# Kernel tuning notes

Measured on AMD Instinct MI355X. Metric: run time of the kernel, lower is better.

## Reference

```python
import jax, jax.numpy as jnp
import numpy as np

# fixed finite-difference stencils (torch cross-correlation taps)
W5 = (1.0/12.0, -8.0/12.0, 0.0, 8.0/12.0, -1.0/12.0)  # five-point, pad=2
W3 = (-0.5, 0.0, 0.5)                                   # three-point, pad=1
P_LIST = np.array([10.0, 8.5, 5.0], dtype=np.float32).reshape(3, 1, 1)


def _circ_deriv(x, axis, taps, pad):
    # torch conv with circular pad: out[i] = sum_k w[k] * x[(i + k - pad) % n]
    # x[(i + k - pad) % n] == roll(x, pad - k)[i]
    out = jnp.zeros_like(x)
    for k, w in enumerate(taps):
        if w != 0.0:
            out = out + w * jnp.roll(x, pad - k, axis=axis)
    return out


def setup_inputs() -> dict:
    key = jax.random.key(0)
    k1, k2, k3, k4 = jax.random.split(key, 4)
    b, si_z, i_y, i_x = 4, 12, 720, 1440
    return {
        "Field": jax.random.normal(k1, (b, si_z, i_y, i_x), dtype=jnp.float32),
        "W": jax.random.normal(k2, (15, 12), dtype=jnp.float32) * 0.02,
        "b_bias": jax.random.normal(k3, (15,), dtype=jnp.float32) * 0.02,
        "thermal_factor": jax.random.normal(k4, (1,), dtype=jnp.float32),
    }


def reference(Field, W, b_bias, thermal_factor):
    b, si_z, i_y, i_x = Field.shape
    s = 4
    i_z = si_z // s  # == 3

    # backbone: 1x1 conv / channel-mixing linear, (b,12,y,x) -> (b,15,y,x)
    ml = jnp.einsum("oc,bcyx->boyx", W, Field) + b_bias[None, :, None, None]
    ml = ml.reshape(b, s + 1, i_z, i_y, i_x)
    ExternalForce = ml[:, :4]           # (b,4,z,y,x)
    o = ml[:, 4:5]                      # (b,1,z,y,x)

    F5 = Field.reshape(b, s, i_z, i_y, i_x)
    u = F5[:, 0:1]
    v = F5[:, 1:2]
    T = F5[:, 2:3]

    Fdx = _circ_deriv(F5, -1, W5, 2)    # d/dx, circular five-point
    Fdy = _circ_deriv(F5, -2, W5, 2)    # d/dy
    Fdz = _circ_deriv(F5, -3, W3, 1)    # d/dz, three-point

    p_list = jnp.asarray(P_LIST)        # (3,1,1) broadcasts over z,y,x
    term3 = thermal_factor[0] * T[:, 0] / p_list * o[:, 0]   # (b,3,y,x)... (b,z=3,y,x)
    phys = jnp.stack([-Fdx[:, 3], -Fdy[:, 3], term3], axis=1)  # (b,3,z,y,x)
    phys = jnp.pad(phys, ((0, 0), (0, 1), (0, 0), (0, 0), (0, 0)))  # -> (b,4,z,y,x)

    xydirection = -u * Fdx - v * Fdy
    PhysicsPart = xydirection - o * Fdz + phys
    Delta = ExternalForce + PhysicsPart
    Field_new = F5 + Delta

    constrain = Fdx[:, 0] + Fdy[:, 1] + _circ_deriv(o[:, 0], -3, W3, 1)

    return (
        Field_new.reshape(b, si_z, i_y, i_x),
        jnp.mean(constrain ** 2),
        jnp.mean(ExternalForce ** 2),
        jnp.mean(PhysicsPart ** 2),
        jnp.mean(xydirection ** 2),
    )
```

## Files before the change

### kernel.cpp

```cpp
#include <hip/hip_runtime.h>

#define IX 1440
#define IY 720
#define NB 4
#define PLANE (IY * IX)
#define NOUT (NB * 12 * PLANE)
#define TX 32
#define TY 16
#define NBX (IX / TX)
#define NBY (IY / TY)
#define NWG (NB * NBX * NBY)
#define SWZ_Q (NWG / 8)
#define SWZ_R (NWG % 8)
#define HROWS (TY + 4)
#define HCOLS 40
#define TILE4 (HROWS * HCOLS / 4)

typedef float f2v __attribute__((ext_vector_type(2)));
typedef float f4v __attribute__((ext_vector_type(4)));

__global__ void zero_ws_kernel(double* ws) {
    if (threadIdx.x < 4) ws[threadIdx.x] = 0.0;
}

__device__ __forceinline__ void ld2(const float* p, float o[2]) {
    const f2v v = *reinterpret_cast<const f2v*>(p);
    o[0] = v.x; o[1] = v.y;
}

__global__ __launch_bounds__(256) void euler_kernel(
    const float* __restrict__ Field,
    const float* __restrict__ W,
    const float* __restrict__ bvec,
    const float* __restrict__ thermal,
    float* __restrict__ out,
    double* __restrict__ ws)
{
    __shared__ float sW[180];
    __shared__ float sB[16];
    __shared__ f4v  buf4[2][TILE4];
    __shared__ float sRed[4][4];

    const int t = threadIdx.x;
    if (t < 180) sW[t] = W[t];
    if (t < 15)  sB[t] = bvec[t];
    const float th = thermal[0];

    const int bid = blockIdx.x;
    const int xcd = bid & 7, pos = bid >> 3;
    const int wg  = (xcd < SWZ_R ? xcd * (SWZ_Q + 1)
                                 : SWZ_R * (SWZ_Q + 1) + (xcd - SWZ_R) * SWZ_Q) + pos;

    const int bx  = wg % NBX;
    const int tmp = wg / NBX;
    const int by  = tmp % NBY;
    const int b   = tmp / NBY;
    const int x0  = bx * TX, y0 = by * TY;

    const float* base = Field + (size_t)b * 12 * PLANE;

    const bool ldact = (t < TILE4);
    int loff = 0;
    if (ldact) {
        const int r = t / 10, q = t % 10;
        int gy = y0 + r - 2;  if (gy < 0) gy += IY; else if (gy >= IY) gy -= IY;
        int gx = x0 - 4 + q * 4; if (gx < 0) gx += IX; else if (gx >= IX) gx -= IX;
        loff = gy * IX + gx;
    }

    const int ty  = t >> 4, txi = t & 15;
    const int yl  = ty + 2;
    const int xl  = 4 + 2 * txi;
    const size_t po = (size_t)(y0 + ty) * IX + (x0 + 2 * txi);

    constexpr int ORD[12] = {9, 0, 3, 6, 10, 1, 4, 7, 11, 2, 5, 8};

    float ctr[12][2];
#pragma unroll
    for (int c = 0; c < 12; ++c) ld2(base + (size_t)c * PLANE + po, ctr[c]);

    f4v r0 = {};
    if (ldact) r0 = *reinterpret_cast<const f4v*>(base + (size_t)9 * PLANE + loff);

    __syncthreads();

    float ml12[3][2];
#pragma unroll
    for (int z = 0; z < 3; ++z) {
#pragma unroll
        for (int j = 0; j < 2; ++j) ml12[z][j] = sB[12 + z];
#pragma unroll
        for (int cc = 0; cc < 12; ++cc) {
            const float wv = sW[(12 + z) * 12 + cc];
#pragma unroll
            for (int j = 0; j < 2; ++j) ml12[z][j] = fmaf(wv, ctr[cc][j], ml12[z][j]);
        }
    }

    if (ldact) buf4[0][t] = r0;
    __syncthreads();

    float c2 = 0.f, ef2 = 0.f, pp2 = 0.f, xy2 = 0.f;
    float fdx9[2], fdy9[2], conz[2];
    float* ob = out + (size_t)b * 12 * PLANE + po;

#pragma unroll
    for (int ci = 0; ci < 12; ++ci) {
        const int c  = ORD[ci];
        const int f  = c / 3, z = c % 3;
        const int zp = (z == 2) ? 0 : z + 1;
        const int zm = (z == 0) ? 2 : z - 1;
        const float invp = (z == 0) ? 0.1f : (z == 1) ? (1.0f / 8.5f) : 0.2f;

        f4v rn = {};
        if (ci < 11 && ldact)
            rn = *reinterpret_cast<const f4v*>(base + (size_t)ORD[ci + 1] * PLANE + loff);

        const float* fb = reinterpret_cast<const float*>(buf4[ci & 1]);

        const f2v wa = *reinterpret_cast<const f2v*>(&fb[yl * HCOLS + xl - 2]);
        const f2v wb = *reinterpret_cast<const f2v*>(&fb[yl * HCOLS + xl]);
        const f2v wc = *reinterpret_cast<const f2v*>(&fb[yl * HCOLS + xl + 2]);
        const f2v m2 = *reinterpret_cast<const f2v*>(&fb[(yl - 2) * HCOLS + xl]);
        const f2v m1 = *reinterpret_cast<const f2v*>(&fb[(yl - 1) * HCOLS + xl]);
        const f2v p1 = *reinterpret_cast<const f2v*>(&fb[(yl + 1) * HCOLS + xl]);
        const f2v p2 = *reinterpret_cast<const f2v*>(&fb[(yl + 2) * HCOLS + xl]);

        float fdx[2], fdy[2];
        fdx[0] = (wa.x - wc.x + 8.0f * (wb.y - wa.y)) * (1.0f / 12.0f);
        fdx[1] = (wa.y - wc.y + 8.0f * (wc.x - wb.x)) * (1.0f / 12.0f);
        fdy[0] = (m2.x - p2.x + 8.0f * (p1.x - m1.x)) * (1.0f / 12.0f);
        fdy[1] = (m2.y - p2.y + 8.0f * (p1.y - m1.y)) * (1.0f / 12.0f);

        float mlc[2];
#pragma unroll
        for (int j = 0; j < 2; ++j) mlc[j] = sB[c];
#pragma unroll
        for (int cc = 0; cc < 12; ++cc) {
            const float wv = sW[c * 12 + cc];
#pragma unroll
            for (int j = 0; j < 2; ++j) mlc[j] = fmaf(wv, ctr[cc][j], mlc[j]);
        }

        if (f == 3) {
#pragma unroll
            for (int j = 0; j < 2; ++j) {
                fdx9[j] = fdx[j]; fdy9[j] = fdy[j];
                conz[j] = 0.5f * (ml12[zp][j] - ml12[zm][j]);
            }
        }
        if (f == 0) {
#pragma unroll
            for (int j = 0; j < 2; ++j) conz[j] += fdx[j];
        }
        if (f == 1) {
#pragma unroll
            for (int j = 0; j < 2; ++j) conz[j] += fdy[j];
        }

        float st[2];
#pragma unroll
        for (int j = 0; j < 2; ++j) {
            const float fdz = 0.5f * (ctr[f * 3 + zp][j] - ctr[f * 3 + zm][j]);
            const float xyd = -ctr[z][j] * fdx[j] - ctr[3 + z][j] * fdy[j];
            float ph;
            if      (f == 0) ph = -fdx9[j];
            else if (f == 1) ph = -fdy9[j];
            else if (f == 2) ph = th * ctr[6 + z][j] * invp * ml12[z][j];
            else             ph = 0.0f;
            const float phys = xyd - ml12[z][j] * fdz + ph;
            st[j] = ctr[c][j] + mlc[j] + phys;
            ef2 = fmaf(mlc[j], mlc[j], ef2);
            pp2 = fmaf(phys,   phys,   pp2);
            xy2 = fmaf(xyd,    xyd,    xy2);
        }
        f2v sv; sv.x = st[0]; sv.y = st[1];
        __builtin_nontemporal_store(sv, reinterpret_cast<f2v*>(ob + (size_t)c * PLANE));

        if (f == 2) {
#pragma unroll
            for (int j = 0; j < 2; ++j) c2 = fmaf(conz[j], conz[j], c2);
        }

        if (ci < 11) {
            if (ldact) buf4[(ci + 1) & 1][t] = rn;
            __syncthreads();
        }
    }

    float vals[4] = { c2, ef2, pp2, xy2 };
    const int lane = t & 63;
    const int wv   = t >> 6;
#pragma unroll
    for (int i = 0; i < 4; ++i) {
        float v = vals[i];
        for (int off = 32; off > 0; off >>= 1) v += __shfl_down(v, off, 64);
        if (lane == 0) sRed[wv][i] = v;
    }
    __syncthreads();
    if (t < 4) {
        const double s = (double)sRed[0][t] + (double)sRed[1][t]
                       + (double)sRed[2][t] + (double)sRed[3][t];
        atomicAdd(&ws[t], s);
    }
}

__global__ void finalize_kernel(const double* __restrict__ ws, float* __restrict__ out) {
    if (threadIdx.x == 0) {
        out[NOUT + 0] = (float)(ws[0] / (double)(NB * 3 * PLANE));
        out[NOUT + 1] = (float)(ws[1] / (double)NOUT);
        out[NOUT + 2] = (float)(ws[2] / (double)NOUT);
        out[NOUT + 3] = (float)(ws[3] / (double)NOUT);
    }
}

extern "C" void kernel_launch(void* const* d_in, const int* in_sizes, int n_in,
                              void* d_out, int out_size, void* d_ws, size_t ws_size,
                              hipStream_t stream) {
    const float* Field   = (const float*)d_in[0];
    const float* W       = (const float*)d_in[1];
    const float* bvec    = (const float*)d_in[2];
    const float* thermal = (const float*)d_in[3];
    float*  out = (float*)d_out;
    double* ws  = (double*)d_ws;

    zero_ws_kernel<<<1, 64, 0, stream>>>(ws);
    euler_kernel<<<NWG, 256, 0, stream>>>(Field, W, bvec, thermal, out, ws);
    finalize_kernel<<<1, 64, 0, stream>>>(ws, out);
}
```

Baseline: 127.1 us.

## Stage all twelve channel halo tiles in LDS with one up-front load batch

Replaces the double-buffered, per-channel halo pipeline with a single batch that issues all twelve float4 halo loads at once, writes them into a 12-channel LDS tile and synchronises once. The centre values are then read from LDS instead of separate global loads, and the eleven per-channel barriers are removed. The goal is more memory-level parallelism and less barrier overhead. In exchange, LDS use grows to about 38 KB per block and register pressure rises from holding 12 float4 values, which may reduce occupancy.

```diff
diff --git a/kernel.cpp b/kernel.cpp
--- a/kernel.cpp
+++ b/kernel.cpp
@@ -14,18 +14,14 @@
 #define SWZ_R (NWG % 8)
 #define HROWS (TY + 4)
 #define HCOLS 40
-#define TILE4 (HROWS * HCOLS / 4)
+#define TILEF (HROWS * HCOLS)
+#define TILE4 (TILEF / 4)
 
 typedef float f2v __attribute__((ext_vector_type(2)));
 typedef float f4v __attribute__((ext_vector_type(4)));
 
 __global__ void zero_ws_kernel(double* ws) {
     if (threadIdx.x < 4) ws[threadIdx.x] = 0.0;
-}
-
-__device__ __forceinline__ void ld2(const float* p, float o[2]) {
-    const f2v v = *reinterpret_cast<const f2v*>(p);
-    o[0] = v.x; o[1] = v.y;
 }
 
 __global__ __launch_bounds__(256) void euler_kernel(
@@ -36,9 +32,9 @@
     float* __restrict__ out,
     double* __restrict__ ws)
 {
+    __shared__ float tile[12][TILEF];
     __shared__ float sW[180];
     __shared__ float sB[16];
-    __shared__ f4v  buf4[2][TILE4];
     __shared__ float sRed[4][4];
 
     const int t = threadIdx.x;
@@ -60,29 +56,38 @@
     const float* base = Field + (size_t)b * 12 * PLANE;
 
     const bool ldact = (t < TILE4);
-    int loff = 0;
+    size_t goff = 0;
     if (ldact) {
         const int r = t / 10, q = t % 10;
-        int gy = y0 + r - 2;  if (gy < 0) gy += IY; else if (gy >= IY) gy -= IY;
+        int gy = y0 + r - 2;     if (gy < 0) gy += IY; else if (gy >= IY) gy -= IY;
         int gx = x0 - 4 + q * 4; if (gx < 0) gx += IX; else if (gx >= IX) gx -= IX;
-        loff = gy * IX + gx;
-    }
+        goff = (size_t)gy * IX + gx;
+    }
+    f4v rg[12];
+    if (ldact) {
+#pragma unroll
+        for (int c = 0; c < 12; ++c)
+            rg[c] = *reinterpret_cast<const f4v*>(base + (size_t)c * PLANE + goff);
+    }
+    __builtin_amdgcn_sched_barrier(0);
+    if (ldact) {
+#pragma unroll
+        for (int c = 0; c < 12; ++c)
+            *reinterpret_cast<f4v*>(&tile[c][t * 4]) = rg[c];
+    }
+    __syncthreads();
 
     const int ty  = t >> 4, txi = t & 15;
-    const int yl  = ty + 2;
+    const int rb  = (ty + 2) * HCOLS;
     const int xl  = 4 + 2 * txi;
     const size_t po = (size_t)(y0 + ty) * IX + (x0 + 2 * txi);
 
-    constexpr int ORD[12] = {9, 0, 3, 6, 10, 1, 4, 7, 11, 2, 5, 8};
-
     float ctr[12][2];
 #pragma unroll
-    for (int c = 0; c < 12; ++c) ld2(base + (size_t)c * PLANE + po, ctr[c]);
-
-    f4v r0 = {};
-    if (ldact) r0 = *reinterpret_cast<const f4v*>(base + (size_t)9 * PLANE + loff);
-
-    __syncthreads();
+    for (int c = 0; c < 12; ++c) {
+        const f2v v = *reinterpret_cast<const f2v*>(&tile[c][rb + xl]);
+        ctr[c][0] = v.x; ctr[c][1] = v.y;
+    }
 
     float ml12[3][2];
 #pragma unroll
@@ -97,95 +102,84 @@
         }
     }
 
-    if (ldact) buf4[0][t] = r0;
-    __syncthreads();
-
     float c2 = 0.f, ef2 = 0.f, pp2 = 0.f, xy2 = 0.f;
-    float fdx9[2], fdy9[2], conz[2];
     float* ob = out + (size_t)b * 12 * PLANE + po;
 
 #pragma unroll
-    for (int ci = 0; ci < 12; ++ci) {
-        const int c  = ORD[ci];
-        const int f  = c / 3, z = c % 3;
+    for (int z = 0; z < 3; ++z) {
         const int zp = (z == 2) ? 0 : z + 1;
         const int zm = (z == 0) ? 2 : z - 1;
         const float invp = (z == 0) ? 0.1f : (z == 1) ? (1.0f / 8.5f) : 0.2f;
 
-        f4v rn = {};
-        if (ci < 11 && ldact)
-            rn = *reinterpret_cast<const f4v*>(base + (size_t)ORD[ci + 1] * PLANE + loff);
-
-        const float* fb = reinterpret_cast<const float*>(buf4[ci & 1]);
-
-        const f2v wa = *reinterpret_cast<const f2v*>(&fb[yl * HCOLS + xl - 2]);
-        const f2v wb = *reinterpret_cast<const f2v*>(&fb[yl * HCOLS + xl]);
-        const f2v wc = *reinterpret_cast<const f2v*>(&fb[yl * HCOLS + xl + 2]);
-        const f2v m2 = *reinterpret_cast<const f2v*>(&fb[(yl - 2) * HCOLS + xl]);
-        const f2v m1 = *reinterpret_cast<const f2v*>(&fb[(yl - 1) * HCOLS + xl]);
-        const f2v p1 = *reinterpret_cast<const f2v*>(&fb[(yl + 1) * HCOLS + xl]);
-        const f2v p2 = *reinterpret_cast<const f2v*>(&fb[(yl + 2) * HCOLS + xl]);
-
-        float fdx[2], fdy[2];
-        fdx[0] = (wa.x - wc.x + 8.0f * (wb.y - wa.y)) * (1.0f / 12.0f);
-        fdx[1] = (wa.y - wc.y + 8.0f * (wc.x - wb.x)) * (1.0f / 12.0f);
-        fdy[0] = (m2.x - p2.x + 8.0f * (p1.x - m1.x)) * (1.0f / 12.0f);
-        fdy[1] = (m2.y - p2.y + 8.0f * (p1.y - m1.y)) * (1.0f / 12.0f);
-
-        float mlc[2];
-#pragma unroll
-        for (int j = 0; j < 2; ++j) mlc[j] = sB[c];
-#pragma unroll
-        for (int cc = 0; cc < 12; ++cc) {
-            const float wv = sW[c * 12 + cc];
-#pragma unroll
-            for (int j = 0; j < 2; ++j) mlc[j] = fmaf(wv, ctr[cc][j], mlc[j]);
+        float fdx9[2], fdy9[2], conz[2];
+
+#pragma unroll
+        for (int fi = 0; fi < 4; ++fi) {
+            const int f = (fi == 0) ? 3 : fi - 1;
+            const int c = f * 3 + z;
+            const float* tl = tile[c];
+
+            const f2v wa = *reinterpret_cast<const f2v*>(&tl[rb + xl - 2]);
+            const f2v wc = *reinterpret_cast<const f2v*>(&tl[rb + xl + 2]);
+            const f2v m2 = *reinterpret_cast<const f2v*>(&tl[rb - 2 * HCOLS + xl]);
+            const f2v m1 = *reinterpret_cast<const f2v*>(&tl[rb - 1 * HCOLS + xl]);
+            const f2v p1 = *reinterpret_cast<const f2v*>(&tl[rb + 1 * HCOLS + xl]);
+            const f2v p2 = *reinterpret_cast<const f2v*>(&tl[rb + 2 * HCOLS + xl]);
+
+            float fdx[2], fdy[2];
+            fdx[0] = (wa.x - wc.x + 8.0f * (ctr[c][1] - wa.y)) * (1.0f / 12.0f);
+            fdx[1] = (wa.y - wc.y + 8.0f * (wc.x - ctr[c][0])) * (1.0f / 12.0f);
+            fdy[0] = (m2.x - p2.x + 8.0f * (p1.x - m1.x)) * (1.0f / 12.0f);
+            fdy[1] = (m2.y - p2.y + 8.0f * (p1.y - m1.y)) * (1.0f / 12.0f);
+
+            float mlc[2];
+#pragma unroll
+            for (int j = 0; j < 2; ++j) mlc[j] = sB[c];
+#pragma unroll
+            for (int cc = 0; cc < 12; ++cc) {
+                const float wv = sW[c * 12 + cc];
+#pragma unroll
+                for (int j = 0; j < 2; ++j) mlc[j] = fmaf(wv, ctr[cc][j], mlc[j]);
+            }
+
+            if (f == 3) {
+#pragma unroll
+                for (int j = 0; j < 2; ++j) {
+                    fdx9[j] = fdx[j]; fdy9[j] = fdy[j];
+                    conz[j] = 0.5f * (ml12[zp][j] - ml12[zm][j]);
+                }
+            }
+            if (f == 0) {
+#pragma unroll
+                for (int j = 0; j < 2; ++j) conz[j] += fdx[j];
+            }
+            if (f == 1) {
+#pragma unroll
+                for (int j = 0; j < 2; ++j) conz[j] += fdy[j];
+            }
+
+            float st[2];
+#pragma unroll
+            for (int j = 0; j < 2; ++j) {
+                const float fdz = 0.5f * (ctr[f * 3 + zp][j] - ctr[f * 3 + zm][j]);
+                const float xyd = -ctr[z][j] * fdx[j] - ctr[3 + z][j] * fdy[j];
+                float ph;
+                if      (f == 0) ph = -fdx9[j];
+                else if (f == 1) ph = -fdy9[j];
+                else if (f == 2) ph = th * ctr[6 + z][j] * invp * ml12[z][j];
+                else             ph = 0.0f;
+                const float phys = xyd - ml12[z][j] * fdz + ph;
+                st[j] = ctr[c][j] + mlc[j] + phys;
+                ef2 = fmaf(mlc[j], mlc[j], ef2);
+                pp2 = fmaf(phys,   phys,   pp2);
+                xy2 = fmaf(xyd,    xyd,    xy2);
+            }
+            f2v sv; sv.x = st[0]; sv.y = st[1];
+            __builtin_nontemporal_store(sv, reinterpret_cast<f2v*>(ob + (size_t)c * PLANE));
         }
 
-        if (f == 3) {
-#pragma unroll
-            for (int j = 0; j < 2; ++j) {
-                fdx9[j] = fdx[j]; fdy9[j] = fdy[j];
-                conz[j] = 0.5f * (ml12[zp][j] - ml12[zm][j]);
-            }
-        }
-        if (f == 0) {
-#pragma unroll
-            for (int j = 0; j < 2; ++j) conz[j] += fdx[j];
-        }
-        if (f == 1) {
-#pragma unroll
-            for (int j = 0; j < 2; ++j) conz[j] += fdy[j];
-        }
-
-        float st[2];
-#pragma unroll
-        for (int j = 0; j < 2; ++j) {
-            const float fdz = 0.5f * (ctr[f * 3 + zp][j] - ctr[f * 3 + zm][j]);
-            const float xyd = -ctr[z][j] * fdx[j] - ctr[3 + z][j] * fdy[j];
-            float ph;
-            if      (f == 0) ph = -fdx9[j];
-            else if (f == 1) ph = -fdy9[j];
-            else if (f == 2) ph = th * ctr[6 + z][j] * invp * ml12[z][j];
-            else             ph = 0.0f;
-            const float phys = xyd - ml12[z][j] * fdz + ph;
-            st[j] = ctr[c][j] + mlc[j] + phys;
-            ef2 = fmaf(mlc[j], mlc[j], ef2);
-            pp2 = fmaf(phys,   phys,   pp2);
-            xy2 = fmaf(xyd,    xyd,    xy2);
-        }
-        f2v sv; sv.x = st[0]; sv.y = st[1];
-        __builtin_nontemporal_store(sv, reinterpret_cast<f2v*>(ob + (size_t)c * PLANE));
-
-        if (f == 2) {
-#pragma unroll
-            for (int j = 0; j < 2; ++j) c2 = fmaf(conz[j], conz[j], c2);
-        }
-
-        if (ci < 11) {
-            if (ldact) buf4[(ci + 1) & 1][t] = rn;
-            __syncthreads();
-        }
+#pragma unroll
+        for (int j = 0; j < 2; ++j) c2 = fmaf(conz[j], conz[j], c2);
     }
 
     float vals[4] = { c2, ef2, pp2, xy2 };
```

Measured after the change: 131.3 us. 1.03x slower.
